# Performance work log

Measured on AMD Instinct MI355X. Metric: run time of the kernel, lower is better.

The kernel has to match this reference:

```python
import jax, jax.numpy as jnp
import numpy as np

MU = 0.9
IN_DIM = 1024
OUT_DIM = 8192
N = 8192


def setup_inputs() -> dict:
    key = jax.random.key(0)
    ks = jax.random.split(key, 8)
    stdv = 1.0 / np.sqrt(IN_DIM)
    inp = {
        "x": jax.random.normal(ks[0], (N, IN_DIM), dtype=jnp.float32),
        "x_ctx": jax.random.normal(ks[1], (N, IN_DIM), dtype=jnp.float32),
        "labels": jax.random.randint(ks[2], (N,), 0, OUT_DIM, dtype=jnp.int64),
        # classifier: uniform(-stdv, stdv), shape [output_dim, input_dim]
        "classifier": jax.random.uniform(ks[3], (OUT_DIM, IN_DIM), dtype=jnp.float32, minval=-stdv, maxval=stdv),
        # ctx_q = Linear(input_dim, output_dim - 1)  (na_att=False)
        "ctx_q_w": jax.random.uniform(ks[4], (OUT_DIM - 1, IN_DIM), dtype=jnp.float32, minval=-stdv, maxval=stdv),
        "ctx_q_b": jnp.zeros((OUT_DIM - 1,), dtype=jnp.float32),
        # word_g = Linear(input_dim, 1)
        "word_g_w": jax.random.uniform(ks[5], (1, IN_DIM), dtype=jnp.float32, minval=-stdv, maxval=stdv),
        "word_g_b": jnp.zeros((1,), dtype=jnp.float32),
        # registered buffers, initialized to zero as in __init__
        "history_input": jnp.zeros((OUT_DIM - 1, IN_DIM), dtype=jnp.float32),
        "history_count": jnp.zeros((OUT_DIM - 1,), dtype=jnp.int64),
    }
    return inp


def reference(x, x_ctx, labels, classifier, ctx_q_w, ctx_q_b, word_g_w, word_g_b,
              history_input, history_count):
    # ---- update_history: fused segment-mean EMA (replaces python loop over classes) ----
    xs = jax.lax.stop_gradient(x)  # .clone().detach() in torch
    sums = jax.ops.segment_sum(xs, labels, num_segments=OUT_DIM)          # [C, D]
    cnts = jax.ops.segment_sum(jnp.ones((N,), xs.dtype), labels, num_segments=OUT_DIM)  # [C]
    means = sums / jnp.maximum(cnts, 1.0)[:, None]                        # per-class mean
    present = cnts[1:] > 0                                                # classes 1..C-1
    new_hist = jnp.where(present[:, None], MU * history_input + means[1:], history_input)
    new_count = history_count + present.astype(history_count.dtype)

    # ---- generate_substitute ----
    w_logits = x_ctx @ ctx_q_w.T + ctx_q_b                                # [N, C-1]
    w = jax.nn.softmax(w_logits, axis=-1)
    clamped = jnp.maximum(new_count, 1).astype(x.dtype)
    v = new_hist * (1.0 - MU) / (1.0 - jnp.power(MU, clamped))[:, None]   # bias-corrected EMA
    substitute = w @ v                                                    # [N, D]

    # ---- gated mix + classifier logits ----
    g = jax.nn.sigmoid(x @ word_g_w.T + word_g_b)                         # [N, 1]
    feat = g * x + (1.0 - g) * substitute
    logits = feat @ classifier.T                                          # [N, C]

    # ---- cross_entropy over labels >= 0 (masked mean, jit-safe) ----
    mask = labels >= 0
    logp = jax.nn.log_softmax(logits, axis=-1)
    safe_lbl = jnp.maximum(labels, 0)
    nll = -jnp.take_along_axis(logp, safe_lbl[:, None], axis=1)[:, 0]
    loss = jnp.sum(jnp.where(mask, nll, 0.0)) / jnp.maximum(jnp.sum(mask), 1).astype(nll.dtype)
    return loss, logits
```

## Files before the change

### kernel.cpp

```cpp
#include <hip/hip_runtime.h>
#include <hip/hip_bf16.h>
#include <cstddef>
#include <cstdint>

typedef __hip_bfloat16 bf16;
typedef float floatx4 __attribute__((ext_vector_type(4)));
typedef short shortx8 __attribute__((ext_vector_type(8)));

#define NROWS 8192
#define INDIM 1024
#define OUTDIM 8192
#define CM1 8191

__device__ __forceinline__ void gload16(const void* g, void* l) {
  __builtin_amdgcn_global_load_lds(
      (const __attribute__((address_space(1))) void*)g,
      (__attribute__((address_space(3))) void*)l, 16, 0, 0);
}

__global__ __launch_bounds__(256) void seg_acc_kernel(
    const float* __restrict__ x, const int* __restrict__ labels,
    float* __restrict__ sums, int* __restrict__ cnts) {
  int i = blockIdx.x;
  int l = labels[i];
  const float* xr = x + (size_t)i * INDIM;
  float* sr = sums + (size_t)l * INDIM;
  for (int d = threadIdx.x; d < INDIM; d += 256) atomicAdd(&sr[d], xr[d]);
  if (threadIdx.x == 0) atomicAdd(&cnts[l], 1);
}

__global__ __launch_bounds__(256) void cvt8_kernel(
    const float* __restrict__ in, bf16* __restrict__ out, long n_in, long n_out) {
  long i = ((long)blockIdx.x * 256 + threadIdx.x) * 8;
  if (i >= n_out) return;
  shortx8 o;
  if (i + 8 <= n_in) {
    floatx4 a = *(const floatx4*)(in + i);
    floatx4 b = *(const floatx4*)(in + i + 4);
#pragma unroll
    for (int j = 0; j < 4; j++) {
      o[j] = __builtin_bit_cast(short, __float2bfloat16(a[j]));
      o[j + 4] = __builtin_bit_cast(short, __float2bfloat16(b[j]));
    }
  } else {
#pragma unroll
    for (int j = 0; j < 8; j++) o[j] = 0;
  }
  *(shortx8*)(out + i) = o;
}

__global__ __launch_bounds__(256) void make_vt_kernel(
    const float* __restrict__ sums, const int* __restrict__ cnts,
    const float* __restrict__ hist, const int* __restrict__ hist_cnt,
    bf16* __restrict__ vT) {
  __shared__ float tile[64][65];
  __shared__ float scl[64];
  __shared__ float rc[64];
  __shared__ int prs[64];
  const int t = threadIdx.x;
  const int cb = blockIdx.x & 127;
  const int db = blockIdx.x >> 7;
  const int c0 = cb * 64, d0 = db * 64;

  if (t < 64) {
    int c = c0 + t;
    float scale = 0.f, rcnt = 0.f;
    int present = 0;
    if (c < CM1) {
      int cnt = cnts[c + 1];
      present = cnt > 0;
      rcnt = 1.0f / fmaxf((float)cnt, 1.0f);
      int nc = hist_cnt[c] + (present ? 1 : 0);
      float clamped = (float)(nc > 1 ? nc : 1);
      scale = 0.1f / (1.0f - powf(0.9f, clamped));
    }
    scl[t] = scale;
    rc[t] = rcnt;
    prs[t] = present;
  }
  __syncthreads();

  const int dl = t & 63;
  const int cl0 = t >> 6;
#pragma unroll
  for (int ii = 0; ii < 16; ii++) {
    int clc = cl0 * 16 + ii;
    int c = c0 + clc;
    float val = 0.f;
    if (c < CM1) {
      float mean = sums[(size_t)(c + 1) * INDIM + d0 + dl] * rc[clc];
      float h = hist[(size_t)c * INDIM + d0 + dl];
      float nh = prs[clc] ? (0.9f * h + mean) : h;
      val = nh * scl[clc];
    }
    tile[clc][dl] = val;
  }
  __syncthreads();

  const int clw = t & 63;
  const int dl0 = t >> 6;
#pragma unroll
  for (int jj = 0; jj < 16; jj++) {
    int dlc = dl0 * 16 + jj;
    vT[(size_t)(d0 + dlc) * OUTDIM + c0 + clw] = __float2bfloat16(tile[clw][dlc]);
  }
}

__device__ __forceinline__ void store_c(float* p, float v) { *p = v; }
__device__ __forceinline__ void store_c(bf16* p, float v) { *p = __float2bfloat16(v); }

template <typename OutT>
__global__ __launch_bounds__(256) void gemm_bt_kernel(
    const bf16* __restrict__ A, const bf16* __restrict__ B, OutT* __restrict__ C,
    int K, int ldc) {
  __shared__ bf16 As[128 * 64];
  __shared__ bf16 Bs[128 * 64];
  const int t = threadIdx.x;
  const int lane = t & 63;
  const int wave = t >> 6;

  const int bm = blockIdx.y * 128;
  const int bn = blockIdx.x * 128;

  const int wm = (wave >> 1) * 64;
  const int wn = (wave & 1) * 64;
  const int r = lane & 15;
  const int q = lane >> 4;
  const int wbase = t & 192;

  floatx4 acc[4][4];
#pragma unroll
  for (int i = 0; i < 4; i++)
#pragma unroll
    for (int j = 0; j < 4; j++) acc[i][j] = (floatx4){0.f, 0.f, 0.f, 0.f};

  for (int k0 = 0; k0 < K; k0 += 64) {
#pragma unroll
    for (int i = 0; i < 4; i++) {
      int c = i * 256 + t;
      int row = c >> 3;
      int gc = ((c & 7) ^ (row & 7)) << 3;
      gload16(A + (size_t)(bm + row) * K + k0 + gc, &As[(i * 256 + wbase) * 8]);
      gload16(B + (size_t)(bn + row) * K + k0 + gc, &Bs[(i * 256 + wbase) * 8]);
    }
    __syncthreads();
#pragma unroll
    for (int kk = 0; kk < 64; kk += 32) {
      shortx8 af[4], bfr[4];
      const int pc = ((kk >> 3) + q) ^ (r & 7);
#pragma unroll
      for (int i = 0; i < 4; i++) {
        af[i] = *(const shortx8*)(&As[(wm + i * 16 + r) * 64 + pc * 8]);
        bfr[i] = *(const shortx8*)(&Bs[(wn + i * 16 + r) * 64 + pc * 8]);
      }
#pragma unroll
      for (int i = 0; i < 4; i++)
#pragma unroll
        for (int j = 0; j < 4; j++)
          acc[i][j] = __builtin_amdgcn_mfma_f32_16x16x32_bf16(af[i], bfr[j], acc[i][j], 0, 0, 0);
    }
    __syncthreads();
  }

#pragma unroll
  for (int i = 0; i < 4; i++)
#pragma unroll
    for (int j = 0; j < 4; j++)
#pragma unroll
      for (int rr = 0; rr < 4; rr++) {
        int m = bm + wm + i * 16 + q * 4 + rr;
        int n = bn + wn + j * 16 + r;
        store_c(&C[(size_t)m * ldc + n], acc[i][j][rr]);
      }
}

__global__ __launch_bounds__(256) void softmax_rows_kernel(
    bf16* __restrict__ wl, const float* __restrict__ bias) {
  __shared__ float red[4];
  const int t = threadIdx.x;
  bf16* p = wl + (size_t)blockIdx.x * OUTDIM;
  float vals[32];
  float mx = -1e30f;
#pragma unroll
  for (int i = 0; i < 32; i++) {
    int col = i * 256 + t;
    float v = -1e30f;
    if (col < CM1) v = __bfloat162float(p[col]) + bias[col];
    vals[i] = v;
    mx = fmaxf(mx, v);
  }
  for (int o = 32; o; o >>= 1) mx = fmaxf(mx, __shfl_down(mx, o, 64));
  if ((t & 63) == 0) red[t >> 6] = mx;
  __syncthreads();
  mx = fmaxf(fmaxf(red[0], red[1]), fmaxf(red[2], red[3]));
  __syncthreads();
  float s = 0.f;
#pragma unroll
  for (int i = 0; i < 32; i++) {
    int col = i * 256 + t;
    float e = (col < CM1) ? __expf(vals[i] - mx) : 0.f;
    vals[i] = e;
    s += e;
  }
  for (int o = 32; o; o >>= 1) s += __shfl_down(s, o, 64);
  if ((t & 63) == 0) red[t >> 6] = s;
  __syncthreads();
  s = red[0] + red[1] + red[2] + red[3];
  float rs = 1.0f / s;
#pragma unroll
  for (int i = 0; i < 32; i++) {
    int col = i * 256 + t;
    p[col] = __float2bfloat16(vals[i] * rs);
  }
}

__global__ __launch_bounds__(256) void g_feat_kernel(
    const float* __restrict__ x, const float* __restrict__ wg,
    const float* __restrict__ wgb, const bf16* __restrict__ sub,
    bf16* __restrict__ feat) {
  __shared__ float red[4];
  const int t = threadIdx.x;
  const float* xr = x + (size_t)blockIdx.x * INDIM;
  float dot = 0.f;
#pragma unroll
  for (int i = 0; i < 4; i++) {
    int d = i * 256 + t;
    dot += xr[d] * wg[d];
  }
  for (int o = 32; o; o >>= 1) dot += __shfl_down(dot, o, 64);
  if ((t & 63) == 0) red[t >> 6] = dot;
  __syncthreads();
  dot = red[0] + red[1] + red[2] + red[3];
  float g = 1.0f / (1.0f + __expf(-(dot + wgb[0])));
  const bf16* sr = sub + (size_t)blockIdx.x * INDIM;
  bf16* fr = feat + (size_t)blockIdx.x * INDIM;
#pragma unroll
  for (int i = 0; i < 4; i++) {
    int d = i * 256 + t;
    float f = g * xr[d] + (1.0f - g) * __bfloat162float(sr[d]);
    fr[d] = __float2bfloat16(f);
  }
}

__global__ __launch_bounds__(256) void ce_kernel(
    const float* __restrict__ logits, const int* __restrict__ labels,
    float* __restrict__ acc) {
  __shared__ float red[4];
  const int t = threadIdx.x;
  const float* p = logits + (size_t)blockIdx.x * OUTDIM;
  float vals[32];
  float mx = -1e30f;
#pragma unroll
  for (int i = 0; i < 32; i++) {
    float v = p[i * 256 + t];
    vals[i] = v;
    mx = fmaxf(mx, v);
  }
  for (int o = 32; o; o >>= 1) mx = fmaxf(mx, __shfl_down(mx, o, 64));
  if ((t & 63) == 0) red[t >> 6] = mx;
  __syncthreads();
  mx = fmaxf(fmaxf(red[0], red[1]), fmaxf(red[2], red[3]));
  __syncthreads();
  float s = 0.f;
#pragma unroll
  for (int i = 0; i < 32; i++) s += __expf(vals[i] - mx);
  for (int o = 32; o; o >>= 1) s += __shfl_down(s, o, 64);
  if ((t & 63) == 0) red[t >> 6] = s;
  __syncthreads();
  if (t == 0) {
    s = red[0] + red[1] + red[2] + red[3];
    int l = labels[blockIdx.x];
    if (l >= 0) {
      float nll = mx + logf(s) - p[l];
      atomicAdd(&acc[0], nll);
      atomicAdd(&acc[1], 1.0f);
    }
  }
}

__global__ void finalize_kernel(const float* __restrict__ acc, float* __restrict__ out) {
  out[0] = acc[0] / fmaxf(acc[1], 1.0f);
}

extern "C" void kernel_launch(void* const* d_in, const int* in_sizes, int n_in,
                              void* d_out, int out_size, void* d_ws, size_t ws_size,
                              hipStream_t stream) {
  const float* x        = (const float*)d_in[0];
  const float* x_ctx    = (const float*)d_in[1];
  const int*   labels   = (const int*)d_in[2];
  const float* cls      = (const float*)d_in[3];
  const float* ctxq_w   = (const float*)d_in[4];
  const float* ctxq_b   = (const float*)d_in[5];
  const float* wg_w     = (const float*)d_in[6];
  const float* wg_b     = (const float*)d_in[7];
  const float* hist     = (const float*)d_in[8];
  const int*   hist_cnt = (const int*)d_in[9];
  float* out = (float*)d_out;

  char* ws = (char*)d_ws;
  float* sums   = (float*)(ws + 0);
  int*   cnts   = (int*)  (ws + 33554432);
  float* acc    = (float*)(ws + 33587200);
  bf16* xctx_bf = (bf16*) (ws + 33587456);
  bf16* wq_bf   = (bf16*) (ws + 50364672);
  bf16* cls_bf  = (bf16*) (ws + 67141888);
  bf16* vT      = (bf16*) (ws + 83919104);
  bf16* wl      = (bf16*) (ws + 100696320);
  bf16* sub_bf  = (bf16*) (ws + 234914048);
  bf16* feat_bf = (bf16*) (ws + 251691264);

  hipMemsetAsync(ws, 0, 33587456 + 256, stream);

  seg_acc_kernel<<<NROWS, 256, 0, stream>>>(x, labels, sums, cnts);
  cvt8_kernel<<<4096, 256, 0, stream>>>(x_ctx, xctx_bf, (long)NROWS * INDIM,
                                        (long)NROWS * INDIM);
  cvt8_kernel<<<4096, 256, 0, stream>>>(ctxq_w, wq_bf, (long)CM1 * INDIM,
                                        (long)OUTDIM * INDIM);
  cvt8_kernel<<<4096, 256, 0, stream>>>(cls, cls_bf, (long)OUTDIM * INDIM,
                                        (long)OUTDIM * INDIM);
  make_vt_kernel<<<2048, 256, 0, stream>>>(sums, cnts, hist, hist_cnt, vT);

  gemm_bt_kernel<bf16><<<dim3(64, 64), 256, 0, stream>>>(xctx_bf, wq_bf, wl, 1024, OUTDIM);
  softmax_rows_kernel<<<NROWS, 256, 0, stream>>>(wl, ctxq_b);
  gemm_bt_kernel<bf16><<<dim3(8, 64), 256, 0, stream>>>(wl, vT, sub_bf, OUTDIM, INDIM);
  g_feat_kernel<<<NROWS, 256, 0, stream>>>(x, wg_w, wg_b, sub_bf, feat_bf);
  gemm_bt_kernel<float><<<dim3(64, 64), 256, 0, stream>>>(feat_bf, cls_bf, out + 1, 1024, OUTDIM);
  ce_kernel<<<NROWS, 256, 0, stream>>>(out + 1, labels, acc);
  finalize_kernel<<<1, 1, 0, stream>>>(acc, out);
}
```

Before: 1.185 ms.

## Add double-buffered 256x256-tile GEMM for the two K=1024 projections

Adds a new GEMM kernel with 256x256 output tiles, 512 threads, double-buffered LDS staging and an LDS-staged vectorized bf16 epilogue. It is used for the context-query logits GEMM and the classifier logits GEMM. The larger tiles raise data reuse per global load, and the double buffering overlaps the next tile's loads with the current MFMA work. In exchange it uses 128KB of LDS per block and many accumulator registers, which lowers occupancy to one block per CU. The grid also shrinks to 1024 blocks.

```diff
diff --git a/kernel.cpp b/kernel.cpp
--- a/kernel.cpp
+++ b/kernel.cpp
@@ -137,7 +137,7 @@
   for (int k0 = 0; k0 < K; k0 += 64) {
 #pragma unroll
     for (int i = 0; i < 4; i++) {
-      int c = i * 256 + t;
+      int c = t + i * 256;
       int row = c >> 3;
       int gc = ((c & 7) ^ (row & 7)) << 3;
       gload16(A + (size_t)(bm + row) * K + k0 + gc, &As[(i * 256 + wbase) * 8]);
@@ -172,6 +172,111 @@
         int n = bn + wn + j * 16 + r;
         store_c(&C[(size_t)m * ldc + n], acc[i][j][rr]);
       }
+}
+
+template <typename OutT>
+__global__ __launch_bounds__(512) void gemm256_kernel(
+    const bf16* __restrict__ A, const bf16* __restrict__ B, OutT* __restrict__ C,
+    int K, int ldc) {
+  __shared__ bf16 As[2][256 * 64];
+  __shared__ bf16 Bs[2][256 * 64];
+  const int t = threadIdx.x;
+  const int lane = t & 63;
+  const int wave = t >> 6;
+  const int bm = blockIdx.y * 256;
+  const int bn = blockIdx.x * 256;
+  const int wr = (wave >> 2) * 128;
+  const int wc = (wave & 3) * 64;
+  const int r = lane & 15;
+  const int q = lane >> 4;
+
+  floatx4 acc[8][4];
+#pragma unroll
+  for (int i = 0; i < 8; i++)
+#pragma unroll
+    for (int j = 0; j < 4; j++) acc[i][j] = (floatx4){0.f, 0.f, 0.f, 0.f};
+
+#define STAGE256(sel, kk0)                                                        \
+  {                                                                               \
+    _Pragma("unroll") for (int i = 0; i < 4; i++) {                               \
+      int c = i * 512 + t;                                                        \
+      int row = c >> 3;                                                           \
+      int gc = ((c & 7) ^ (row & 7)) << 3;                                        \
+      gload16(A + (size_t)(bm + row) * K + (kk0) + gc,                            \
+              &As[sel][(i * 512 + wave * 64) * 8]);                               \
+      gload16(B + (size_t)(bn + row) * K + (kk0) + gc,                            \
+              &Bs[sel][(i * 512 + wave * 64) * 8]);                               \
+    }                                                                             \
+  }
+
+#define COMPUTE256(sel)                                                           \
+  {                                                                               \
+    _Pragma("unroll") for (int kk = 0; kk < 64; kk += 32) {                       \
+      shortx8 bfr[4];                                                             \
+      _Pragma("unroll") for (int j = 0; j < 4; j++) {                             \
+        int br = wc + j * 16 + r;                                                 \
+        bfr[j] = *(const shortx8*)(&Bs[sel][br * 64 +                             \
+                                           ((((kk >> 3) + q) ^ (br & 7)) << 3)]); \
+      }                                                                           \
+      _Pragma("unroll") for (int i = 0; i < 8; i++) {                             \
+        int ar = wr + i * 16 + r;                                                 \
+        shortx8 af = *(const shortx8*)(&As[sel][ar * 64 +                         \
+                                           ((((kk >> 3) + q) ^ (ar & 7)) << 3)]); \
+        _Pragma("unroll") for (int j = 0; j < 4; j++)                             \
+          acc[i][j] =                                                             \
+              __builtin_amdgcn_mfma_f32_16x16x32_bf16(af, bfr[j], acc[i][j], 0, 0, 0); \
+      }                                                                           \
+    }                                                                             \
+  }
+
+  const int nk = K >> 6;
+  STAGE256(0, 0);
+  __syncthreads();
+  for (int kt = 0; kt < nk - 2; kt += 2) {
+    STAGE256(1, (kt + 1) * 64);
+    COMPUTE256(0);
+    __syncthreads();
+    STAGE256(0, (kt + 2) * 64);
+    COMPUTE256(1);
+    __syncthreads();
+  }
+  STAGE256(1, (nk - 1) * 64);
+  COMPUTE256(0);
+  __syncthreads();
+  COMPUTE256(1);
+
+  if constexpr (sizeof(OutT) == 2) {
+    __syncthreads();
+    bf16* slab = ((bf16*)As) + wave * 1024;
+    const int lr = lane >> 2;
+    const int lc = (lane & 3) * 16;
+#pragma unroll
+    for (int i = 0; i < 8; i++) {
+#pragma unroll
+      for (int j = 0; j < 4; j++)
+#pragma unroll
+        for (int rr = 0; rr < 4; rr++)
+          slab[(q * 4 + rr) * 64 + j * 16 + r] = __float2bfloat16(acc[i][j][rr]);
+      shortx8 v0 = *(const shortx8*)(&slab[lr * 64 + lc]);
+      shortx8 v1 = *(const shortx8*)(&slab[lr * 64 + lc + 8]);
+      OutT* crow = C + (size_t)(bm + wr + i * 16 + lr) * ldc + bn + wc + lc;
+      *(shortx8*)crow = v0;
+      *(shortx8*)(crow + 8) = v1;
+    }
+  } else {
+#pragma unroll
+    for (int i = 0; i < 8; i++)
+#pragma unroll
+      for (int j = 0; j < 4; j++)
+#pragma unroll
+        for (int rr = 0; rr < 4; rr++) {
+          int m = bm + wr + i * 16 + q * 4 + rr;
+          int n = bn + wc + j * 16 + r;
+          C[(size_t)m * ldc + n] = acc[i][j][rr];
+        }
+  }
+#undef STAGE256
+#undef COMPUTE256
 }
 
 __global__ __launch_bounds__(256) void softmax_rows_kernel(
@@ -320,11 +425,11 @@
                                         (long)OUTDIM * INDIM);
   make_vt_kernel<<<2048, 256, 0, stream>>>(sums, cnts, hist, hist_cnt, vT);
 
-  gemm_bt_kernel<bf16><<<dim3(64, 64), 256, 0, stream>>>(xctx_bf, wq_bf, wl, 1024, OUTDIM);
+  gemm256_kernel<bf16><<<dim3(32, 32), 512, 0, stream>>>(xctx_bf, wq_bf, wl, 1024, OUTDIM);
   softmax_rows_kernel<<<NROWS, 256, 0, stream>>>(wl, ctxq_b);
   gemm_bt_kernel<bf16><<<dim3(8, 64), 256, 0, stream>>>(wl, vT, sub_bf, OUTDIM, INDIM);
   g_feat_kernel<<<NROWS, 256, 0, stream>>>(x, wg_w, wg_b, sub_bf, feat_bf);
-  gemm_bt_kernel<float><<<dim3(64, 64), 256, 0, stream>>>(feat_bf, cls_bf, out + 1, 1024, OUTDIM);
+  gemm256_kernel<float><<<dim3(32, 32), 512, 0, stream>>>(feat_bf, cls_bf, out + 1, 1024, OUTDIM);
   ce_kernel<<<NROWS, 256, 0, stream>>>(out + 1, labels, acc);
   finalize_kernel<<<1, 1, 0, stream>>>(acc, out);
 }
```

Result: no change. 1.180 ms (-0.4%).
